# Performance work log

Hardware: AMD Instinct MI355X
Metric: run time of the kernel (lower is better)

The kernel has to match this reference:

```python
import jax, jax.numpy as jnp
import numpy as np

EPS = 1e-7
ALPHA = 16.0
RANK = 64
CURV = 1.0


def lorentz_expmap0(x, c):
    # x: [N, d] tangent at origin (spatial part). Returns [N, d+1] point on hyperboloid.
    sc = jnp.sqrt(c)
    vn = jnp.maximum(jnp.linalg.norm(x, axis=-1, keepdims=True), EPS)  # [N,1]
    t = jnp.cosh(sc * vn) / sc                                        # [N,1] time coord
    sp = (jnp.sinh(sc * vn) / (sc * vn)) * x                          # [N,d] spatial
    return jnp.concatenate([t, sp], axis=-1)


def lorentz_recompute_time(s, c):
    # s: [N, d] spatial part. time = sqrt(1/c + ||s||^2) so <p,p>_L = -1/c.
    sq = jnp.sum(s * s, axis=-1, keepdims=True)
    t = jnp.sqrt(1.0 / c + sq)
    return jnp.concatenate([t, s], axis=-1)


def lorentz_logmap0(p, c):
    # p: [N, d+1] on hyperboloid. Returns [N, d] tangent (spatial) at origin.
    sc = jnp.sqrt(c)
    t = p[:, :1]
    y = p[:, 1:]
    yn = jnp.maximum(jnp.linalg.norm(y, axis=-1, keepdims=True), EPS)
    arg = jnp.maximum(sc * t, 1.0 + EPS)  # arccosh domain clamp
    d = jnp.arccosh(arg) / sc             # geodesic distance from origin
    return (d / yn) * y


def setup_inputs() -> dict:
    key = jax.random.key(0)
    k1, k2, k3 = jax.random.split(key, 3)
    N, D_IN, D_OUT, R = 16384, 4096, 4096, RANK
    x = jax.random.normal(k1, (N, D_IN), dtype=jnp.float32) * 0.02
    # torch Linear weight layout: A_w [r, in], B_w [out, r]
    A_w = jax.random.normal(k2, (R, D_IN), dtype=jnp.float32) * (1.0 / np.sqrt(D_IN))
    B_w = jax.random.normal(k3, (D_OUT, R), dtype=jnp.float32) * (1.0 / np.sqrt(R))
    return {"x": x, "A_w": A_w, "B_w": B_w}


def reference(x, A_w, B_w):
    c = CURV
    p0 = lorentz_expmap0(x, c)                    # [N, D_IN+1]
    s1 = p0[:, 1:] @ A_w.T                        # [N, R]
    p1 = lorentz_recompute_time(s1, c)            # [N, R+1]
    s2 = p1[:, 1:] @ B_w.T                        # [N, D_OUT]
    p2 = lorentz_recompute_time(s2, c)            # [N, D_OUT+1]
    v = lorentz_logmap0(p2, c)                    # [N, D_OUT]
    return (ALPHA / RANK) * v
```

## Files before the change

kernel.cpp:

```cpp
#include <hip/hip_runtime.h>
#include <hip/hip_bf16.h>

#define NROWS 16384
#define DIN   4096
#define DOUT  4096
#define RNK   64
#define EPSF  1e-7f

typedef float  f32x4  __attribute__((ext_vector_type(4)));
typedef __bf16 bf16x4 __attribute__((ext_vector_type(4)));
typedef __bf16 bf16x8 __attribute__((ext_vector_type(8)));

__device__ __forceinline__ bf16x8 cvt8(f32x4 a, f32x4 b) {
    bf16x8 r;
    r[0]=(__bf16)a.x; r[1]=(__bf16)a.y; r[2]=(__bf16)a.z; r[3]=(__bf16)a.w;
    r[4]=(__bf16)b.x; r[5]=(__bf16)b.y; r[6]=(__bf16)b.z; r[7]=(__bf16)b.w;
    return r;
}

__global__ __launch_bounds__(512, 4)
void kb_gram(const float* __restrict__ Bw, __bf16* __restrict__ Bpf,
             float* __restrict__ Gpart) {
    __shared__ __bf16 bs[256][72];
    const int t = threadIdx.x;
    const int jb = blockIdx.x * 256;

    {
        const int j0 = t >> 1, c0 = (t & 1) * 32;
        #pragma unroll
        for (int u = 0; u < 4; ++u) {
            f32x4 v0 = *(const f32x4*)&Bw[(size_t)(jb + j0) * RNK + c0 + 8*u];
            f32x4 v1 = *(const f32x4*)&Bw[(size_t)(jb + j0) * RNK + c0 + 8*u + 4];
            *(bf16x8*)&bs[j0][c0 + 8*u] = cvt8(v0, v1);
        }
    }
    __syncthreads();

    #pragma unroll
    for (int u = 0; u < 4; ++u) {
        const int lc = t + 512 * u;
        const int ll = lc & 63;
        const int ks = (lc >> 6) & 1;
        const int jl = lc >> 7;
        bf16x8 v = *(const bf16x8*)&bs[jl * 16 + (ll & 15)][ks * 32 + (ll >> 4) * 8];
        const size_t C = ((size_t)((jb >> 4) + jl) * 2 + ks) * 64 + ll;
        *(bf16x8*)&Bpf[C * 8] = v;
    }

    const int r = t & 63, rp = (t >> 6) * 8;
    float acc[8] = {0,0,0,0,0,0,0,0};
    for (int j = 0; j < 256; ++j) {
        float s = (float)bs[j][r];
        bf16x8 v = *(const bf16x8*)&bs[j][rp];
        #pragma unroll
        for (int u = 0; u < 8; ++u) acc[u] += s * (float)v[u];
    }
    #pragma unroll
    for (int u = 0; u < 8; ++u)
        Gpart[(size_t)blockIdx.x * 4096 + r * 64 + rp + u] = acc[u];
}

__global__ void kc0_sum(const float* __restrict__ Gpart, float* __restrict__ G) {
    const int t = threadIdx.x;
    #pragma unroll
    for (int v = 0; v < 4; ++v) {
        f32x4 a = {0.f, 0.f, 0.f, 0.f};
        for (int b = 0; b < 16; ++b)
            a += *(const f32x4*)&Gpart[(size_t)b * 4096 + t * 16 + v * 4];
        *(f32x4*)&G[t * 16 + v * 4] = a;
    }
}

#define LPK 136
__global__ __launch_bounds__(512, 4)
void kfused(const float* __restrict__ x, const float* __restrict__ Aw,
            const float* __restrict__ G, const __bf16* __restrict__ Bpf,
            float* __restrict__ out) {
    __shared__ __bf16 xs[32][LPK];
    __shared__ __bf16 as[64][LPK];
    __shared__ float  Gs[64][64];
    __shared__ float  s1f[32][64];
    __shared__ __bf16 s1pf[2][2][64][8];
    __shared__ float  rowss[32];
    __shared__ float  gs[32];

    const int t = threadIdx.x;
    const int l = t & 63;
    const int w = t >> 6;
    const int brow = blockIdx.x * 32;

    {
        float* gf = &Gs[0][0];
        *(f32x4*)&gf[t * 8]     = *(const f32x4*)&G[t * 8];
        *(f32x4*)&gf[t * 8 + 4] = *(const f32x4*)&G[t * 8 + 4];
    }

    const int xrow = t >> 4, xcol = (t & 15) * 8;
    const int arow = t >> 3, acol = (t & 7) * 16;
    const size_t xb = (size_t)(brow + xrow) * DIN + xcol;
    const size_t ab = (size_t)arow * DIN + acol;

    const int m0   = (w & 1) * 16;
    const int n0   = (w >> 1) * 16;
    const int frow = l & 15;
    const int koff = (l >> 4) * 8;

    float ssq = 0.f;
    f32x4 acc = {0.f, 0.f, 0.f, 0.f};
    f32x4 xA0,xA1,aA0,aA1,aA2,aA3, xB0,xB1,aB0,aB1,aB2,aB3;

    auto load = [&](f32x4&x0,f32x4&x1,f32x4&A0,f32x4&A1,f32x4&A2,f32x4&A3,int kt){
        const size_t o = (size_t)kt * 128;
        x0 = *(const f32x4*)&x[xb + o];       x1 = *(const f32x4*)&x[xb + o + 4];
        A0 = *(const f32x4*)&Aw[ab + o];      A1 = *(const f32x4*)&Aw[ab + o + 4];
        A2 = *(const f32x4*)&Aw[ab + o + 8];  A3 = *(const f32x4*)&Aw[ab + o + 12];
    };
    auto consume = [&](const f32x4&x0,const f32x4&x1,const f32x4&A0,
                       const f32x4&A1,const f32x4&A2,const f32x4&A3){
        ssq += x0.x*x0.x + x0.y*x0.y + x0.z*x0.z + x0.w*x0.w;
        ssq += x1.x*x1.x + x1.y*x1.y + x1.z*x1.z + x1.w*x1.w;
        *(bf16x8*)&xs[xrow][xcol]     = cvt8(x0, x1);
        *(bf16x8*)&as[arow][acol]     = cvt8(A0, A1);
        *(bf16x8*)&as[arow][acol + 8] = cvt8(A2, A3);
        __syncthreads();
        #pragma unroll
        for (int ks = 0; ks < 4; ++ks) {
            bf16x8 af  = *(const bf16x8*)&xs[m0 + frow][ks*32 + koff];
            bf16x8 bf_ = *(const bf16x8*)&as[n0 + frow][ks*32 + koff];
            acc = __builtin_amdgcn_mfma_f32_16x16x32_bf16(af, bf_, acc, 0, 0, 0);
        }
        __syncthreads();
    };

    const int NT = DIN / 128;
    load(xA0,xA1,aA0,aA1,aA2,aA3, 0);
    for (int kt = 0; kt < NT; kt += 2) {
        load(xB0,xB1,aB0,aB1,aB2,aB3, kt + 1);
        consume(xA0,xA1,aA0,aA1,aA2,aA3);
        if (kt + 2 < NT) load(xA0,xA1,aA0,aA1,aA2,aA3, kt + 2);
        consume(xB0,xB1,aB0,aB1,aB2,aB3);
    }

    ssq += __shfl_xor(ssq, 1);
    ssq += __shfl_xor(ssq, 2);
    ssq += __shfl_xor(ssq, 4);
    ssq += __shfl_xor(ssq, 8);
    if ((l & 15) == 0) rowss[w * 4 + (l >> 4)] = ssq;
    __syncthreads();
    if (t < 32) {
        float vn = fmaxf(sqrtf(rowss[t]), EPSF);
        rowss[t] = sinhf(vn) / vn;
    }
    __syncthreads();

    #pragma unroll
    for (int q = 0; q < 4; ++q) {
        const int row = m0 + (l >> 4) * 4 + q;
        s1f[row][n0 + frow] = rowss[row] * acc[q];
    }
    __syncthreads();

    {
        const int r0 = w * 4;
        float y0=0.f, y1=0.f, y2=0.f, y3=0.f;
        for (int r = 0; r < 64; ++r) {
            const float gr = Gs[r][l];
            y0 += gr * s1f[r0 + 0][r];
            y1 += gr * s1f[r0 + 1][r];
            y2 += gr * s1f[r0 + 2][r];
            y3 += gr * s1f[r0 + 3][r];
        }
        float q0 = s1f[r0 + 0][l] * y0;
        float q1 = s1f[r0 + 1][l] * y1;
        float q2 = s1f[r0 + 2][l] * y2;
        float q3 = s1f[r0 + 3][l] * y3;
        #pragma unroll
        for (int s = 1; s < 64; s <<= 1) {
            q0 += __shfl_xor(q0, s);
            q1 += __shfl_xor(q1, s);
            q2 += __shfl_xor(q2, s);
            q3 += __shfl_xor(q3, s);
        }
        if (l == 0) {
            float r2v[4] = {q0, q1, q2, q3};
            #pragma unroll
            for (int i = 0; i < 4; ++i) {
                const float r2 = r2v[i];
                const float rn = sqrtf(r2);
                gs[r0 + i] = 0.25f * acoshf(fmaxf(sqrtf(1.f + r2), 1.f + EPSF))
                                   / fmaxf(rn, EPSF);
            }
        }
    }
    __syncthreads();

    if (t < 256) {
        const int ll = t & 63, ksq = (t >> 6) & 1, mg = t >> 7;
        const int row = mg * 16 + (ll & 15);
        const int kc  = ksq * 32 + (ll >> 4) * 8;
        const float gg = gs[row];
        bf16x8 p;
        #pragma unroll
        for (int u = 0; u < 8; ++u) p[u] = (__bf16)(gg * s1f[row][kc + u]);
        *(bf16x8*)&s1pf[mg][ksq][ll][0] = p;
    }
    __syncthreads();

    {
        const int mg = w & 1;
        const int mr0 = mg * 16;
        const bf16x8 a0f = *(const bf16x8*)&s1pf[mg][0][l][0];
        const bf16x8 a1f = *(const bf16x8*)&s1pf[mg][1][l][0];
        #pragma unroll 4
        for (int jj = 0; jj < 64; ++jj) {
            const int j = (w >> 1) + jj * 4;
            const size_t base = ((size_t)j * 2 * 64 + l) * 8;
            bf16x8 b0 = *(const bf16x8*)&Bpf[base];
            bf16x8 b1 = *(const bf16x8*)&Bpf[base + 512];
            f32x4 a2 = {0.f, 0.f, 0.f, 0.f};
            a2 = __builtin_amdgcn_mfma_f32_16x16x32_bf16(a0f, b0, a2, 0, 0, 0);
            a2 = __builtin_amdgcn_mfma_f32_16x16x32_bf16(a1f, b1, a2, 0, 0, 0);
            const int col = j * 16 + frow;
            #pragma unroll
            for (int q = 0; q < 4; ++q) {
                const int row = mr0 + (l >> 4) * 4 + q;
                out[(size_t)(brow + row) * DOUT + col] = a2[q];
            }
        }
    }
}

extern "C" void kernel_launch(void* const* d_in, const int* in_sizes, int n_in,
                              void* d_out, int out_size, void* d_ws, size_t ws_size,
                              hipStream_t stream) {
    const float* x  = (const float*)d_in[0];
    const float* Aw = (const float*)d_in[1];
    const float* Bw = (const float*)d_in[2];
    float* out = (float*)d_out;

    char* ws = (char*)d_ws;
    __bf16* Bpf   = (__bf16*)(ws);
    float*  Gpart = (float*)(ws + 524288);
    float*  G     = (float*)(ws + 786432);

    kb_gram<<<16, 512, 0, stream>>>(Bw, Bpf, Gpart);
    kc0_sum<<<1, 256, 0, stream>>>(Gpart, G);
    kfused<<<NROWS / 32, 512, 0, stream>>>(x, Aw, G, Bpf, out);
}
```

Baseline: 182.5 us.

## Split fused kernel into pre-packed A projection and separate output GEMM kernel

Adds a kernel that converts A_w to bf16 in MFMA fragment order, so the first GEMM can read A fragments straight from global memory with register double-buffering and split-K across waves, with no LDS staging or per-step barriers. The first kernel now handles 16 rows per block and writes the scaled s1 fragments to workspace. A second kernel computes the output tile grid with vectorized f32x4 stores. The goal is to remove LDS sync overhead and the strided scalar output writes. The cost is an extra launch and a global round-trip for s1.

```diff
diff --git a/kernel.cpp b/kernel.cpp
--- a/kernel.cpp
+++ b/kernel.cpp
@@ -16,6 +16,20 @@
     r[0]=(__bf16)a.x; r[1]=(__bf16)a.y; r[2]=(__bf16)a.z; r[3]=(__bf16)a.w;
     r[4]=(__bf16)b.x; r[5]=(__bf16)b.y; r[6]=(__bf16)b.z; r[7]=(__bf16)b.w;
     return r;
+}
+__device__ __forceinline__ bf16x4 cvt4(f32x4 v) {
+    bf16x4 r;
+    r[0]=(__bf16)v.x; r[1]=(__bf16)v.y; r[2]=(__bf16)v.z; r[3]=(__bf16)v.w;
+    return r;
+}
+
+__global__ __launch_bounds__(512, 2)
+void ka_apf(const float* __restrict__ Aw, __bf16* __restrict__ Apf) {
+    const int kt = blockIdx.x;
+    const int t = threadIdx.x;
+    const int ng = t >> 7, le = (t >> 1) & 63, h = t & 1;
+    f32x4 v = *(const f32x4*)&Aw[(size_t)(ng*16 + (le&15)) * DIN + kt*32 + (le>>4)*8 + h*4];
+    *(bf16x4*)&Apf[((size_t)(kt*4 + ng))*512 + le*8 + h*4] = cvt4(v);
 }
 
 __global__ __launch_bounds__(512, 4)
@@ -71,163 +85,141 @@
     }
 }
 
-#define LPK 136
-__global__ __launch_bounds__(512, 4)
-void kfused(const float* __restrict__ x, const float* __restrict__ Aw,
-            const float* __restrict__ G, const __bf16* __restrict__ Bpf,
-            float* __restrict__ out) {
-    __shared__ __bf16 xs[32][LPK];
-    __shared__ __bf16 as[64][LPK];
-    __shared__ float  Gs[64][64];
-    __shared__ float  s1f[32][64];
-    __shared__ __bf16 s1pf[2][2][64][8];
-    __shared__ float  rowss[32];
-    __shared__ float  gs[32];
-
-    const int t = threadIdx.x;
-    const int l = t & 63;
-    const int w = t >> 6;
-    const int brow = blockIdx.x * 32;
-
+__global__ __launch_bounds__(256, 4)
+void k1(const float* __restrict__ x, const __bf16* __restrict__ Apf,
+        const float* __restrict__ G, __bf16* __restrict__ s1pf) {
+    __shared__ float part[4][16][68];
+    __shared__ float Gs[64][64];
+    __shared__ float s1s[16][68];
+    __shared__ float ssqs[4][16];
+    __shared__ float gsl[16];
+
+    const int t = threadIdx.x, l = t & 63, w = t >> 6;
+    const int brow = blockIdx.x * 16;
+    const int rl = l & 15, ko = l >> 4;
+
+    const size_t xoff = (size_t)(brow + rl) * DIN + (size_t)w * 1024 + ko * 8;
+    const size_t aoff = (size_t)(w * 32) * 2048 + (size_t)l * 8;
+
+    f32x4 acc0 = {0,0,0,0}, acc1 = {0,0,0,0}, acc2 = {0,0,0,0}, acc3 = {0,0,0,0};
+    float ssq = 0.f;
+
+    f32x4 xc0 = *(const f32x4*)&x[xoff];
+    f32x4 xc1 = *(const f32x4*)&x[xoff + 4];
+    bf16x8 a0 = *(const bf16x8*)&Apf[aoff];
+    bf16x8 a1 = *(const bf16x8*)&Apf[aoff + 512];
+    bf16x8 a2 = *(const bf16x8*)&Apf[aoff + 1024];
+    bf16x8 a3 = *(const bf16x8*)&Apf[aoff + 1536];
+
+    #pragma unroll
+    for (int i = 0; i < 32; ++i) {
+        f32x4 xn0 = xc0, xn1 = xc1;
+        bf16x8 b0 = a0, b1 = a1, b2 = a2, b3 = a3;
+        if (i < 31) {
+            xn0 = *(const f32x4*)&x[xoff + (i+1)*32];
+            xn1 = *(const f32x4*)&x[xoff + (i+1)*32 + 4];
+            const size_t ao = aoff + (size_t)(i+1)*2048;
+            b0 = *(const bf16x8*)&Apf[ao];
+            b1 = *(const bf16x8*)&Apf[ao + 512];
+            b2 = *(const bf16x8*)&Apf[ao + 1024];
+            b3 = *(const bf16x8*)&Apf[ao + 1536];
+        }
+        ssq += xc0.x*xc0.x + xc0.y*xc0.y + xc0.z*xc0.z + xc0.w*xc0.w;
+        ssq += xc1.x*xc1.x + xc1.y*xc1.y + xc1.z*xc1.z + xc1.w*xc1.w;
+        bf16x8 xf = cvt8(xc0, xc1);
+        acc0 = __builtin_amdgcn_mfma_f32_16x16x32_bf16(a0, xf, acc0, 0, 0, 0);
+        acc1 = __builtin_amdgcn_mfma_f32_16x16x32_bf16(a1, xf, acc1, 0, 0, 0);
+        acc2 = __builtin_amdgcn_mfma_f32_16x16x32_bf16(a2, xf, acc2, 0, 0, 0);
+        acc3 = __builtin_amdgcn_mfma_f32_16x16x32_bf16(a3, xf, acc3, 0, 0, 0);
+        xc0 = xn0; xc1 = xn1; a0 = b0; a1 = b1; a2 = b2; a3 = b3;
+    }
+
+    *(f32x4*)&part[w][rl][ 0 + ko*4] = acc0;
+    *(f32x4*)&part[w][rl][16 + ko*4] = acc1;
+    *(f32x4*)&part[w][rl][32 + ko*4] = acc2;
+    *(f32x4*)&part[w][rl][48 + ko*4] = acc3;
+    ssq += __shfl_xor(ssq, 16);
+    ssq += __shfl_xor(ssq, 32);
+    if (l < 16) ssqs[w][l] = ssq;
     {
         float* gf = &Gs[0][0];
-        *(f32x4*)&gf[t * 8]     = *(const f32x4*)&G[t * 8];
-        *(f32x4*)&gf[t * 8 + 4] = *(const f32x4*)&G[t * 8 + 4];
-    }
-
-    const int xrow = t >> 4, xcol = (t & 15) * 8;
-    const int arow = t >> 3, acol = (t & 7) * 16;
-    const size_t xb = (size_t)(brow + xrow) * DIN + xcol;
-    const size_t ab = (size_t)arow * DIN + acol;
-
-    const int m0   = (w & 1) * 16;
-    const int n0   = (w >> 1) * 16;
-    const int frow = l & 15;
-    const int koff = (l >> 4) * 8;
-
-    float ssq = 0.f;
-    f32x4 acc = {0.f, 0.f, 0.f, 0.f};
-    f32x4 xA0,xA1,aA0,aA1,aA2,aA3, xB0,xB1,aB0,aB1,aB2,aB3;
-
-    auto load = [&](f32x4&x0,f32x4&x1,f32x4&A0,f32x4&A1,f32x4&A2,f32x4&A3,int kt){
-        const size_t o = (size_t)kt * 128;
-        x0 = *(const f32x4*)&x[xb + o];       x1 = *(const f32x4*)&x[xb + o + 4];
-        A0 = *(const f32x4*)&Aw[ab + o];      A1 = *(const f32x4*)&Aw[ab + o + 4];
-        A2 = *(const f32x4*)&Aw[ab + o + 8];  A3 = *(const f32x4*)&Aw[ab + o + 12];
-    };
-    auto consume = [&](const f32x4&x0,const f32x4&x1,const f32x4&A0,
-                       const f32x4&A1,const f32x4&A2,const f32x4&A3){
-        ssq += x0.x*x0.x + x0.y*x0.y + x0.z*x0.z + x0.w*x0.w;
-        ssq += x1.x*x1.x + x1.y*x1.y + x1.z*x1.z + x1.w*x1.w;
-        *(bf16x8*)&xs[xrow][xcol]     = cvt8(x0, x1);
-        *(bf16x8*)&as[arow][acol]     = cvt8(A0, A1);
-        *(bf16x8*)&as[arow][acol + 8] = cvt8(A2, A3);
-        __syncthreads();
-        #pragma unroll
-        for (int ks = 0; ks < 4; ++ks) {
-            bf16x8 af  = *(const bf16x8*)&xs[m0 + frow][ks*32 + koff];
-            bf16x8 bf_ = *(const bf16x8*)&as[n0 + frow][ks*32 + koff];
-            acc = __builtin_amdgcn_mfma_f32_16x16x32_bf16(af, bf_, acc, 0, 0, 0);
-        }
-        __syncthreads();
-    };
-
-    const int NT = DIN / 128;
-    load(xA0,xA1,aA0,aA1,aA2,aA3, 0);
-    for (int kt = 0; kt < NT; kt += 2) {
-        load(xB0,xB1,aB0,aB1,aB2,aB3, kt + 1);
-        consume(xA0,xA1,aA0,aA1,aA2,aA3);
-        if (kt + 2 < NT) load(xA0,xA1,aA0,aA1,aA2,aA3, kt + 2);
-        consume(xB0,xB1,aB0,aB1,aB2,aB3);
-    }
-
-    ssq += __shfl_xor(ssq, 1);
-    ssq += __shfl_xor(ssq, 2);
-    ssq += __shfl_xor(ssq, 4);
-    ssq += __shfl_xor(ssq, 8);
-    if ((l & 15) == 0) rowss[w * 4 + (l >> 4)] = ssq;
-    __syncthreads();
-    if (t < 32) {
-        float vn = fmaxf(sqrtf(rowss[t]), EPSF);
-        rowss[t] = sinhf(vn) / vn;
-    }
-    __syncthreads();
-
-    #pragma unroll
-    for (int q = 0; q < 4; ++q) {
-        const int row = m0 + (l >> 4) * 4 + q;
-        s1f[row][n0 + frow] = rowss[row] * acc[q];
-    }
-    __syncthreads();
-
-    {
-        const int r0 = w * 4;
-        float y0=0.f, y1=0.f, y2=0.f, y3=0.f;
-        for (int r = 0; r < 64; ++r) {
-            const float gr = Gs[r][l];
-            y0 += gr * s1f[r0 + 0][r];
-            y1 += gr * s1f[r0 + 1][r];
-            y2 += gr * s1f[r0 + 2][r];
-            y3 += gr * s1f[r0 + 3][r];
-        }
-        float q0 = s1f[r0 + 0][l] * y0;
-        float q1 = s1f[r0 + 1][l] * y1;
-        float q2 = s1f[r0 + 2][l] * y2;
-        float q3 = s1f[r0 + 3][l] * y3;
-        #pragma unroll
-        for (int s = 1; s < 64; s <<= 1) {
-            q0 += __shfl_xor(q0, s);
-            q1 += __shfl_xor(q1, s);
-            q2 += __shfl_xor(q2, s);
-            q3 += __shfl_xor(q3, s);
-        }
-        if (l == 0) {
-            float r2v[4] = {q0, q1, q2, q3};
-            #pragma unroll
-            for (int i = 0; i < 4; ++i) {
-                const float r2 = r2v[i];
-                const float rn = sqrtf(r2);
-                gs[r0 + i] = 0.25f * acoshf(fmaxf(sqrtf(1.f + r2), 1.f + EPSF))
-                                   / fmaxf(rn, EPSF);
-            }
-        }
-    }
-    __syncthreads();
-
-    if (t < 256) {
-        const int ll = t & 63, ksq = (t >> 6) & 1, mg = t >> 7;
-        const int row = mg * 16 + (ll & 15);
-        const int kc  = ksq * 32 + (ll >> 4) * 8;
-        const float gg = gs[row];
+        const float* gp = &G[t * 16];
+        *(f32x4*)&gf[t*16 + 0]  = *(const f32x4*)&gp[0];
+        *(f32x4*)&gf[t*16 + 4]  = *(const f32x4*)&gp[4];
+        *(f32x4*)&gf[t*16 + 8]  = *(const f32x4*)&gp[8];
+        *(f32x4*)&gf[t*16 + 12] = *(const f32x4*)&gp[12];
+    }
+    __syncthreads();
+
+    const int row = t >> 4, c4 = (t & 15) * 4;
+    f32x4 s = *(const f32x4*)&part[0][row][c4];
+    s += *(const f32x4*)&part[1][row][c4];
+    s += *(const f32x4*)&part[2][row][c4];
+    s += *(const f32x4*)&part[3][row][c4];
+    const float ssqt = ssqs[0][row] + ssqs[1][row] + ssqs[2][row] + ssqs[3][row];
+    const float vn = fmaxf(sqrtf(ssqt), EPSF);
+    const float sc = sinhf(vn) / vn;
+    s *= sc;
+    *(f32x4*)&s1s[row][c4] = s;
+    __syncthreads();
+
+    f32x4 yacc = {0,0,0,0};
+    for (int j = 0; j < 64; ++j) {
+        const float sj = s1s[row][j];
+        yacc += *(const f32x4*)&Gs[j][c4] * sj;
+    }
+    float r2p = s.x*yacc.x + s.y*yacc.y + s.z*yacc.z + s.w*yacc.w;
+    r2p += __shfl_xor(r2p, 1);
+    r2p += __shfl_xor(r2p, 2);
+    r2p += __shfl_xor(r2p, 4);
+    r2p += __shfl_xor(r2p, 8);
+    if ((t & 15) == 0) {
+        const float r2 = r2p;
+        const float rn = sqrtf(r2);
+        gsl[row] = 0.25f * acoshf(fmaxf(sqrtf(1.f + r2), 1.f + EPSF))
+                         / fmaxf(rn, EPSF);
+    }
+    __syncthreads();
+
+    if (t < 128) {
+        const int le = t & 63, ks = t >> 6;
+        const int er = le & 15, ec = ks * 32 + (le >> 4) * 8;
+        const float g = gsl[er];
         bf16x8 p;
         #pragma unroll
-        for (int u = 0; u < 8; ++u) p[u] = (__bf16)(gg * s1f[row][kc + u]);
-        *(bf16x8*)&s1pf[mg][ksq][ll][0] = p;
-    }
-    __syncthreads();
-
-    {
-        const int mg = w & 1;
-        const int mr0 = mg * 16;
-        const bf16x8 a0f = *(const bf16x8*)&s1pf[mg][0][l][0];
-        const bf16x8 a1f = *(const bf16x8*)&s1pf[mg][1][l][0];
-        #pragma unroll 4
-        for (int jj = 0; jj < 64; ++jj) {
-            const int j = (w >> 1) + jj * 4;
-            const size_t base = ((size_t)j * 2 * 64 + l) * 8;
-            bf16x8 b0 = *(const bf16x8*)&Bpf[base];
-            bf16x8 b1 = *(const bf16x8*)&Bpf[base + 512];
-            f32x4 a2 = {0.f, 0.f, 0.f, 0.f};
-            a2 = __builtin_amdgcn_mfma_f32_16x16x32_bf16(a0f, b0, a2, 0, 0, 0);
-            a2 = __builtin_amdgcn_mfma_f32_16x16x32_bf16(a1f, b1, a2, 0, 0, 0);
-            const int col = j * 16 + frow;
-            #pragma unroll
-            for (int q = 0; q < 4; ++q) {
-                const int row = mr0 + (l >> 4) * 4 + q;
-                out[(size_t)(brow + row) * DOUT + col] = a2[q];
-            }
-        }
-    }
+        for (int u = 0; u < 8; ++u) p[u] = (__bf16)(g * s1s[er][ec + u]);
+        *(bf16x8*)&s1pf[((size_t)(blockIdx.x * 2 + ks) * 64 + le) * 8] = p;
+    }
+}
+
+__global__ __launch_bounds__(256, 4)
+void k2(const __bf16* __restrict__ s1pf, const __bf16* __restrict__ Bpf,
+        float* __restrict__ out) {
+    const int t = threadIdx.x, l = t & 63, w = t >> 6;
+    const int rt = blockIdx.x >> 6;
+    const int ct = blockIdx.x & 63;
+    const int g16 = rt * 4 + w;
+
+    const bf16x8 sf0 = *(const bf16x8*)&s1pf[((size_t)(g16*2 + 0) * 64 + l) * 8];
+    const bf16x8 sf1 = *(const bf16x8*)&s1pf[((size_t)(g16*2 + 1) * 64 + l) * 8];
+
+    f32x4 acc[4];
+    #pragma unroll
+    for (int ng = 0; ng < 4; ++ng) {
+        const size_t base = ((size_t)((ct*4 + ng)*2) * 64 + l) * 8;
+        bf16x8 b0 = *(const bf16x8*)&Bpf[base];
+        bf16x8 b1 = *(const bf16x8*)&Bpf[base + 512];
+        f32x4 a = {0.f, 0.f, 0.f, 0.f};
+        a = __builtin_amdgcn_mfma_f32_16x16x32_bf16(b0, sf0, a, 0, 0, 0);
+        a = __builtin_amdgcn_mfma_f32_16x16x32_bf16(b1, sf1, a, 0, 0, 0);
+        acc[ng] = a;
+    }
+
+    const int orow = rt * 64 + w * 16 + (l & 15);
+    const size_t ob = (size_t)orow * DOUT + ct * 64 + (l >> 4) * 4;
+    #pragma unroll
+    for (int ng = 0; ng < 4; ++ng)
+        *(f32x4*)&out[ob + ng * 16] = acc[ng];
 }
 
 extern "C" void kernel_launch(void* const* d_in, const int* in_sizes, int n_in,
@@ -239,11 +231,15 @@
     float* out = (float*)d_out;
 
     char* ws = (char*)d_ws;
-    __bf16* Bpf   = (__bf16*)(ws);
-    float*  Gpart = (float*)(ws + 524288);
-    float*  G     = (float*)(ws + 786432);
-
+    __bf16* Apf   = (__bf16*)(ws);
+    __bf16* Bpf   = (__bf16*)(ws + 0x080000);
+    float*  Gpart = (float*)(ws + 0x100000);
+    float*  G     = (float*)(ws + 0x140000);
+    __bf16* s1pf  = (__bf16*)(ws + 0x150000);
+
+    ka_apf<<<128, 512, 0, stream>>>(Aw, Apf);
     kb_gram<<<16, 512, 0, stream>>>(Bw, Bpf, Gpart);
     kc0_sum<<<1, 256, 0, stream>>>(Gpart, G);
-    kfused<<<NROWS / 32, 512, 0, stream>>>(x, Aw, G, Bpf, out);
-}
+    k1<<<NROWS / 16, 256, 0, stream>>>(x, Apf, G, s1pf);
+    k2<<<16384, 256, 0, stream>>>(s1pf, Bpf, out);
+}
```

Result: faster. 178.6 us (-2.1%).
